# Optimization experiments

Hardware: AMD Instinct MI355X
Metric: run time of the kernel (lower is better)

The kernel has to match this reference:

```python
import jax, jax.numpy as jnp
import numpy as np

NUM_ITERS = 3

def squash(t):
    # t: [..., D]; squash along last axis exactly as the torch code:
    # sn * t / ((1+sn) * sqrt(sn))
    sn = jnp.sum(t * t, axis=-1, keepdims=True)
    return sn * t / ((1.0 + sn) * jnp.sqrt(sn))

def setup_inputs() -> dict:
    key = jax.random.key(0)
    k_x, k_w = jax.random.split(key)
    B, O, I, D_out, D_in = 512, 10, 1152, 16, 8
    x = jax.random.normal(k_x, (B, I, D_in), dtype=jnp.float32)
    W = 0.01 * jax.random.normal(k_w, (O, I, D_out, D_in), dtype=jnp.float32)
    return {"x": x, "W": W}

def reference(x, W):
    B = x.shape[0]
    O, I, D_out, _ = W.shape
    # x_hat[b,o,i,d] = sum_e W[o,i,d,e] * x[b,i,e]
    x_hat = jnp.einsum('oide,bie->boid', W, x)          # [B,O,I,D_out]
    x_hat_det = jax.lax.stop_gradient(x_hat)
    b = jnp.zeros((B, O, I), dtype=x.dtype)
    for it in range(NUM_ITERS):
        c = jax.nn.softmax(b, axis=1)                   # over out caps
        if it == NUM_ITERS - 1:
            outputs = squash(jnp.sum(c[:, :, :, None] * x_hat, axis=-2, keepdims=True))
        else:
            outputs = squash(jnp.sum(c[:, :, :, None] * x_hat_det, axis=-2, keepdims=True))
            b = b + jnp.sum(outputs * x_hat_det, axis=-1)
    outputs = jnp.squeeze(outputs, axis=-2)             # [B,O,D_out]
    # decode_idx == -1 branch: pick longest capsule
    classes = jax.nn.softmax(jnp.sqrt(jnp.sum(outputs ** 2, axis=2)), axis=1)  # [B,O]
    idx = jnp.argmax(classes, axis=1)                   # [B]
    masked = jnp.eye(O, dtype=outputs.dtype)[idx]       # [B,O]
    t = jnp.sum(outputs * masked[:, :, None], axis=1)[:, None, :]  # [B,1,D_out]
    return (t, outputs)
```

## Files before the change

kernel.cpp:

```cpp
#include <hip/hip_runtime.h>

#define BB 512
#define OO 10
#define II 1152
#define DD 16
#define EE 8
#define GB 32
#define BOD (BB * OO * DD)
#define WSLAB (II * DD * EE / 4)

typedef float v2f __attribute__((ext_vector_type(2)));
typedef float v4f __attribute__((ext_vector_type(4)));

__device__ __forceinline__ v2f pk_mul(v2f a, v2f b) {
    v2f d;
    asm("v_pk_mul_f32 %0, %1, %2" : "=v"(d) : "v"(a), "v"(b));
    return d;
}
__device__ __forceinline__ v2f pk_fma(v2f a, v2f b, v2f c) {
    v2f d;
    asm("v_pk_fma_f32 %0, %1, %2, %3" : "=v"(d) : "v"(a), "v"(b), "v"(c));
    return d;
}

__device__ __forceinline__ float dot8(v4f wa, v4f wb, v4f xa, v4f xb) {
    v2f p = pk_mul(wa.lo, xa.lo);
    p = pk_fma(wa.hi, xa.hi, p);
    p = pk_fma(wb.lo, xb.lo, p);
    p = pk_fma(wb.hi, xb.hi, p);
    return p.x + p.y;
}

template <int CTRL>
__device__ __forceinline__ float dpp_add(float v) {
    int s = __builtin_amdgcn_update_dpp(0, __float_as_int(v), CTRL, 0xf, 0xf, true);
    return v + __int_as_float(s);
}
__device__ __forceinline__ float dred16(float v) {
    v = dpp_add<0xB1>(v);
    v = dpp_add<0x4E>(v);
    v = dpp_add<0x141>(v);
    v = dpp_add<0x140>(v);
    return v;
}

__device__ __forceinline__ float squash_lane(float sv) {
    float sn = dred16(sv * sv);
    return sv * (sn / ((1.0f + sn) * sqrtf(sn)));
}

template <int PASS, int IC, int MINW, bool ATOMIC>
__global__ __launch_bounds__(256, MINW)
void caps_pass(const float* __restrict__ x, const float* __restrict__ W,
               float* __restrict__ s_out,
               const float* __restrict__ s0, const float* __restrict__ s1) {
    constexpr int ILEN = II / IC;
    constexpr int XROW = ILEN * 2 + 1;
    __shared__ v4f xlds[GB * XROW];

    const int tid = threadIdx.x;
    const int d = tid & 15;
    const int g = tid >> 4;
    const int bg = blockIdx.x & 15;
    const int ic = blockIdx.x >> 4;
    const int b0 = bg * GB + g;
    const int b1 = b0 + 16;
    const int i0 = ic * ILEN;

    const v4f* x4 = (const v4f*)x;
    for (int k = tid; k < GB * ILEN * 2; k += 256) {
        const int gg = k / (ILEN * 2);
        const int rem = k - gg * (ILEN * 2);
        xlds[gg * XROW + rem] =
            x4[(size_t)(bg * GB + gg) * (II * EE / 4) + (size_t)i0 * 2 + rem];
    }

    constexpr float LOG2E = 1.44269504f;
    float vr0[OO], vr1[OO];
    if constexpr (PASS >= 1) {
        #pragma unroll
        for (int o = 0; o < OO; o++) {
            float v = squash_lane(s0[(b0 * OO + o) * DD + d]);
            float w = squash_lane(s0[(b1 * OO + o) * DD + d]);
            if constexpr (PASS == 2) {
                v += squash_lane(s1[(b0 * OO + o) * DD + d]);
                w += squash_lane(s1[(b1 * OO + o) * DD + d]);
            }
            vr0[o] = v * LOG2E;
            vr1[o] = w * LOG2E;
        }
    }
    __syncthreads();

    float sa0[OO], sa1[OO];
    #pragma unroll
    for (int o = 0; o < OO; o++) { sa0[o] = 0.0f; sa1[o] = 0.0f; }

    const v4f* W4 = (const v4f*)W;
    int widx = (i0 * DD + d) * 2;

    for (int ii = 0; ii < ILEN; ii++) {
        const v4f xa0 = xlds[g * XROW + ii * 2 + 0];
        const v4f xb0 = xlds[g * XROW + ii * 2 + 1];
        const v4f xa1 = xlds[(g + 16) * XROW + ii * 2 + 0];
        const v4f xb1 = xlds[(g + 16) * XROW + ii * 2 + 1];

        float xh0[OO], xh1[OO];
        #pragma unroll
        for (int o = 0; o < OO; o++) {
            const v4f wa = W4[o * WSLAB + widx];
            const v4f wb = W4[o * WSLAB + widx + 1];
            xh0[o] = dot8(wa, wb, xa0, xb0);
            xh1[o] = dot8(wa, wb, xa1, xb1);
        }

        if constexpr (PASS == 0) {
            #pragma unroll
            for (int o = 0; o < OO; o++) { sa0[o] += xh0[o]; sa1[o] += xh1[o]; }
        } else {
            float e0[OO], e1[OO];
            float se0 = 0.0f, se1 = 0.0f;
            #pragma unroll
            for (int o = 0; o < OO; o++) {
                e0[o] = __builtin_amdgcn_exp2f(dred16(vr0[o] * xh0[o]));
                e1[o] = __builtin_amdgcn_exp2f(dred16(vr1[o] * xh1[o]));
                se0 += e0[o];
                se1 += e1[o];
            }
            const float inv0 = __builtin_amdgcn_rcpf(se0);
            const float inv1 = __builtin_amdgcn_rcpf(se1);
            #pragma unroll
            for (int o = 0; o < OO; o++) {
                sa0[o] = fmaf(e0[o] * inv0, xh0[o], sa0[o]);
                sa1[o] = fmaf(e1[o] * inv1, xh1[o], sa1[o]);
            }
        }
        widx += DD * 2;
    }

    if constexpr (ATOMIC) {
        const float scale = (PASS == 0) ? 0.1f : 1.0f;
        #pragma unroll
        for (int o = 0; o < OO; o++) {
            atomicAdd(&s_out[(b0 * OO + o) * DD + d], sa0[o] * scale);
            atomicAdd(&s_out[(b1 * OO + o) * DD + d], sa1[o] * scale);
        }
    } else {
        float* P = s_out + (size_t)ic * BOD;
        #pragma unroll
        for (int o = 0; o < OO; o++) {
            P[(b0 * OO + o) * DD + d] = sa0[o];
            P[(b1 * OO + o) * DD + d] = sa1[o];
        }
    }
}

template <int IC>
__global__ __launch_bounds__(256)
void caps_reduce(const float* __restrict__ P, float* __restrict__ s, float scale) {
    const int idx = blockIdx.x * 256 + threadIdx.x;
    float a = 0.0f;
    #pragma unroll 8
    for (int ic = 0; ic < IC; ic++) a += P[(size_t)ic * BOD + idx];
    s[idx] = a * scale;
}

template <int IC, bool FUSED>
__global__ __launch_bounds__(192)
void caps_final(const float* __restrict__ src, float* __restrict__ out) {
    __shared__ float norml[12];
    const int b = blockIdx.x;
    const int tid = threadIdx.x;
    const int d = tid & 15;
    const int o = tid >> 4;

    float v = 0.0f;
    if (o < OO) {
        float sv;
        const int idx = (b * OO + o) * DD + d;
        if constexpr (FUSED) {
            sv = 0.0f;
            #pragma unroll 8
            for (int ic = 0; ic < IC; ic++) sv += src[(size_t)ic * BOD + idx];
        } else {
            sv = src[idx];
        }
        const float sn = dred16(sv * sv);
        v = sv * (sn / ((1.0f + sn) * sqrtf(sn)));
        out[BB * DD + idx] = v;
        if (d == 0) norml[o] = sn;
    }
    __syncthreads();

    int idx = 0;
    float best = norml[0];
    #pragma unroll
    for (int oo = 1; oo < OO; oo++) {
        const float n = norml[oo];
        if (n > best) { best = n; idx = oo; }
    }
    if (o == idx) out[b * DD + d] = v;
}

extern "C" void kernel_launch(void* const* d_in, const int* in_sizes, int n_in,
                              void* d_out, int out_size, void* d_ws, size_t ws_size,
                              hipStream_t stream) {
    const float* x = (const float*)d_in[0];
    const float* W = (const float*)d_in[1];
    float* out = (float*)d_out;

    constexpr int ICP = 128;
    const size_t needP = ((size_t)ICP * BOD + 2 * BOD) * sizeof(float);

    if (ws_size >= needP) {
        float* P  = (float*)d_ws;
        float* s0 = P + (size_t)ICP * BOD;
        float* s1 = s0 + BOD;
        constexpr int NB = 16 * ICP;

        caps_pass<0, ICP, 4, false><<<NB, 256, 0, stream>>>(x, W, P, nullptr, nullptr);
        caps_reduce<ICP><<<BOD / 256, 256, 0, stream>>>(P, s0, 0.1f);
        caps_pass<1, ICP, 4, false><<<NB, 256, 0, stream>>>(x, W, P, s0, nullptr);
        caps_reduce<ICP><<<BOD / 256, 256, 0, stream>>>(P, s1, 1.0f);
        caps_pass<2, ICP, 4, false><<<NB, 256, 0, stream>>>(x, W, P, s0, s1);
        caps_final<ICP, true><<<BB, 192, 0, stream>>>(P, out);
    } else {
        constexpr int ICA = 64;
        float* s0 = (float*)d_ws;
        float* s1 = s0 + BOD;
        float* s2 = s1 + BOD;
        constexpr int NB = 16 * ICA;

        hipMemsetAsync(d_ws, 0, (size_t)3 * BOD * sizeof(float), stream);
        caps_pass<0, ICA, 4, true><<<NB, 256, 0, stream>>>(x, W, s0, nullptr, nullptr);
        caps_pass<1, ICA, 4, true><<<NB, 256, 0, stream>>>(x, W, s1, s0, nullptr);
        caps_pass<2, ICA, 4, true><<<NB, 256, 0, stream>>>(x, W, s2, s0, s1);
        caps_final<1, false><<<BB, 192, 0, stream>>>(s2, out);
    }
}
```

Measured before the change: 271.5 us.

## Stage W slices in LDS and read x directly from global per thread

Restructures the routing pass so each block of 512 threads stages a slice of W (6 input capsules by 10 output capsules) into shared memory in three sub-steps. Each thread handles one batch row, reading x straight from global instead of from LDS. Before, each thread covered two batch rows and read W from global while x sat in LDS. The input split is now 64 chunks of 18 capsules instead of 128 chunks of 9. This halves the partial-sum buffer and reduce traffic, and W reuse across 32 batch rows now goes through LDS. It adds extra block barriers and non-coalesced per-thread x loads.

```diff
diff --git a/kernel.cpp b/kernel.cpp
--- a/kernel.cpp
+++ b/kernel.cpp
@@ -5,9 +5,17 @@
 #define II 1152
 #define DD 16
 #define EE 8
+#define BOD (BB * OO * DD)
+#define WSLABB (II * DD * EE * 4)
+
+#define TPB 512
 #define GB 32
-#define BOD (BB * OO * DD)
-#define WSLAB (II * DD * EE / 4)
+#define ISUB 6
+#define NSUB 3
+#define ILEN (ISUB * NSUB)
+#define ICN (II / ILEN)
+#define NUNITS (OO * ISUB)
+#define WBYTES (NUNITS * 512)
 
 typedef float v2f __attribute__((ext_vector_type(2)));
 typedef float v4f __attribute__((ext_vector_type(4)));
@@ -49,109 +57,98 @@
     return sv * (sn / ((1.0f + sn) * sqrtf(sn)));
 }
 
-template <int PASS, int IC, int MINW, bool ATOMIC>
-__global__ __launch_bounds__(256, MINW)
+template <int PASS, bool ATOMIC>
+__global__ __launch_bounds__(TPB)
 void caps_pass(const float* __restrict__ x, const float* __restrict__ W,
                float* __restrict__ s_out,
                const float* __restrict__ s0, const float* __restrict__ s1) {
-    constexpr int ILEN = II / IC;
-    constexpr int XROW = ILEN * 2 + 1;
-    __shared__ v4f xlds[GB * XROW];
+    __shared__ char wlds[WBYTES];
 
     const int tid = threadIdx.x;
     const int d = tid & 15;
     const int g = tid >> 4;
     const int bg = blockIdx.x & 15;
     const int ic = blockIdx.x >> 4;
-    const int b0 = bg * GB + g;
-    const int b1 = b0 + 16;
+    const int b = bg * GB + g;
     const int i0 = ic * ILEN;
 
-    const v4f* x4 = (const v4f*)x;
-    for (int k = tid; k < GB * ILEN * 2; k += 256) {
-        const int gg = k / (ILEN * 2);
-        const int rem = k - gg * (ILEN * 2);
-        xlds[gg * XROW + rem] =
-            x4[(size_t)(bg * GB + gg) * (II * EE / 4) + (size_t)i0 * 2 + rem];
-    }
-
     constexpr float LOG2E = 1.44269504f;
-    float vr0[OO], vr1[OO];
+    float vr[OO];
     if constexpr (PASS >= 1) {
         #pragma unroll
         for (int o = 0; o < OO; o++) {
-            float v = squash_lane(s0[(b0 * OO + o) * DD + d]);
-            float w = squash_lane(s0[(b1 * OO + o) * DD + d]);
-            if constexpr (PASS == 2) {
-                v += squash_lane(s1[(b0 * OO + o) * DD + d]);
-                w += squash_lane(s1[(b1 * OO + o) * DD + d]);
+            float v = squash_lane(s0[(b * OO + o) * DD + d]);
+            if constexpr (PASS == 2) v += squash_lane(s1[(b * OO + o) * DD + d]);
+            vr[o] = v * LOG2E;
+        }
+    }
+
+    float sacc[OO];
+    #pragma unroll
+    for (int o = 0; o < OO; o++) sacc[o] = 0.0f;
+
+    const char* xrow = (const char*)x + ((size_t)b * II + i0) * (EE * 4);
+
+    for (int s = 0; s < NSUB; s++) {
+        if (s) __syncthreads();
+        {
+            const char* Wg = (const char*)W + (size_t)(i0 + s * ISUB) * 512;
+            for (int k = tid; k < NUNITS * 32; k += TPB) {
+                const int u  = k >> 5;
+                const int o  = u / ISUB;
+                const int ii = u - o * ISUB;
+                const int sl = k & 31;
+                const v4f w = *(const v4f*)(Wg + (size_t)o * WSLABB + ii * 512
+                                            + (sl & 15) * 32 + (sl >> 4) * 16);
+                *(v4f*)(wlds + k * 16) = w;
             }
-            vr0[o] = v * LOG2E;
-            vr1[o] = w * LOG2E;
-        }
-    }
-    __syncthreads();
-
-    float sa0[OO], sa1[OO];
-    #pragma unroll
-    for (int o = 0; o < OO; o++) { sa0[o] = 0.0f; sa1[o] = 0.0f; }
-
-    const v4f* W4 = (const v4f*)W;
-    int widx = (i0 * DD + d) * 2;
-
-    for (int ii = 0; ii < ILEN; ii++) {
-        const v4f xa0 = xlds[g * XROW + ii * 2 + 0];
-        const v4f xb0 = xlds[g * XROW + ii * 2 + 1];
-        const v4f xa1 = xlds[(g + 16) * XROW + ii * 2 + 0];
-        const v4f xb1 = xlds[(g + 16) * XROW + ii * 2 + 1];
-
-        float xh0[OO], xh1[OO];
-        #pragma unroll
-        for (int o = 0; o < OO; o++) {
-            const v4f wa = W4[o * WSLAB + widx];
-            const v4f wb = W4[o * WSLAB + widx + 1];
-            xh0[o] = dot8(wa, wb, xa0, xb0);
-            xh1[o] = dot8(wa, wb, xa1, xb1);
-        }
-
-        if constexpr (PASS == 0) {
-            #pragma unroll
-            for (int o = 0; o < OO; o++) { sa0[o] += xh0[o]; sa1[o] += xh1[o]; }
-        } else {
-            float e0[OO], e1[OO];
-            float se0 = 0.0f, se1 = 0.0f;
+        }
+        __syncthreads();
+
+        const char* xs = xrow + s * ISUB * 32;
+        const char* wd = wlds + (d << 4);
+        #pragma unroll
+        for (int ii = 0; ii < ISUB; ii++) {
+            const v4f xa = *(const v4f*)(xs + ii * 32);
+            const v4f xb = *(const v4f*)(xs + ii * 32 + 16);
+
+            float xh[OO];
             #pragma unroll
             for (int o = 0; o < OO; o++) {
-                e0[o] = __builtin_amdgcn_exp2f(dred16(vr0[o] * xh0[o]));
-                e1[o] = __builtin_amdgcn_exp2f(dred16(vr1[o] * xh1[o]));
-                se0 += e0[o];
-                se1 += e1[o];
+                const v4f wa = *(const v4f*)(wd + (o * ISUB + ii) * 512);
+                const v4f wb = *(const v4f*)(wd + (o * ISUB + ii) * 512 + 256);
+                xh[o] = dot8(wa, wb, xa, xb);
             }
-            const float inv0 = __builtin_amdgcn_rcpf(se0);
-            const float inv1 = __builtin_amdgcn_rcpf(se1);
-            #pragma unroll
-            for (int o = 0; o < OO; o++) {
-                sa0[o] = fmaf(e0[o] * inv0, xh0[o], sa0[o]);
-                sa1[o] = fmaf(e1[o] * inv1, xh1[o], sa1[o]);
+
+            if constexpr (PASS == 0) {
+                #pragma unroll
+                for (int o = 0; o < OO; o++) sacc[o] += xh[o];
+            } else {
+                float e[OO];
+                float se = 0.0f;
+                #pragma unroll
+                for (int o = 0; o < OO; o++) {
+                    e[o] = __builtin_amdgcn_exp2f(dred16(vr[o] * xh[o]));
+                    se += e[o];
+                }
+                const float inv = __builtin_amdgcn_rcpf(se);
+                #pragma unroll
+                for (int o = 0; o < OO; o++)
+                    sacc[o] = fmaf(e[o] * inv, xh[o], sacc[o]);
             }
         }
-        widx += DD * 2;
     }
 
     if constexpr (ATOMIC) {
         const float scale = (PASS == 0) ? 0.1f : 1.0f;
         #pragma unroll
-        for (int o = 0; o < OO; o++) {
-            atomicAdd(&s_out[(b0 * OO + o) * DD + d], sa0[o] * scale);
-            atomicAdd(&s_out[(b1 * OO + o) * DD + d], sa1[o] * scale);
-        }
+        for (int o = 0; o < OO; o++)
+            atomicAdd(&s_out[(b * OO + o) * DD + d], sacc[o] * scale);
     } else {
         float* P = s_out + (size_t)ic * BOD;
         #pragma unroll
-        for (int o = 0; o < OO; o++) {
-            P[(b0 * OO + o) * DD + d] = sa0[o];
-            P[(b1 * OO + o) * DD + d] = sa1[o];
-        }
+        for (int o = 0; o < OO; o++)
+            P[(b * OO + o) * DD + d] = sacc[o];
     }
 }
 
@@ -209,32 +206,29 @@
     const float* W = (const float*)d_in[1];
     float* out = (float*)d_out;
 
-    constexpr int ICP = 128;
-    const size_t needP = ((size_t)ICP * BOD + 2 * BOD) * sizeof(float);
+    constexpr int NB = 16 * ICN;
+    const size_t needP = ((size_t)ICN * BOD + 2 * BOD) * sizeof(float);
 
     if (ws_size >= needP) {
         float* P  = (float*)d_ws;
-        float* s0 = P + (size_t)ICP * BOD;
+        float* s0 = P + (size_t)ICN * BOD;
         float* s1 = s0 + BOD;
-        constexpr int NB = 16 * ICP;
-
-        caps_pass<0, ICP, 4, false><<<NB, 256, 0, stream>>>(x, W, P, nullptr, nullptr);
-        caps_reduce<ICP><<<BOD / 256, 256, 0, stream>>>(P, s0, 0.1f);
-        caps_pass<1, ICP, 4, false><<<NB, 256, 0, stream>>>(x, W, P, s0, nullptr);
-        caps_reduce<ICP><<<BOD / 256, 256, 0, stream>>>(P, s1, 1.0f);
-        caps_pass<2, ICP, 4, false><<<NB, 256, 0, stream>>>(x, W, P, s0, s1);
-        caps_final<ICP, true><<<BB, 192, 0, stream>>>(P, out);
+
+        caps_pass<0, false><<<NB, TPB, 0, stream>>>(x, W, P, nullptr, nullptr);
+        caps_reduce<ICN><<<BOD / 256, 256, 0, stream>>>(P, s0, 0.1f);
+        caps_pass<1, false><<<NB, TPB, 0, stream>>>(x, W, P, s0, nullptr);
+        caps_reduce<ICN><<<BOD / 256, 256, 0, stream>>>(P, s1, 1.0f);
+        caps_pass<2, false><<<NB, TPB, 0, stream>>>(x, W, P, s0, s1);
+        caps_final<ICN, true><<<BB, 192, 0, stream>>>(P, out);
     } else {
-        constexpr int ICA = 64;
         float* s0 = (float*)d_ws;
         float* s1 = s0 + BOD;
         float* s2 = s1 + BOD;
-        constexpr int NB = 16 * ICA;
 
         hipMemsetAsync(d_ws, 0, (size_t)3 * BOD * sizeof(float), stream);
-        caps_pass<0, ICA, 4, true><<<NB, 256, 0, stream>>>(x, W, s0, nullptr, nullptr);
-        caps_pass<1, ICA, 4, true><<<NB, 256, 0, stream>>>(x, W, s1, s0, nullptr);
-        caps_pass<2, ICA, 4, true><<<NB, 256, 0, stream>>>(x, W, s2, s0, s1);
+        caps_pass<0, true><<<NB, TPB, 0, stream>>>(x, W, s0, nullptr, nullptr);
+        caps_pass<1, true><<<NB, TPB, 0, stream>>>(x, W, s1, s0, nullptr);
+        caps_pass<2, true><<<NB, TPB, 0, stream>>>(x, W, s2, s0, s1);
         caps_final<1, false><<<BB, 192, 0, stream>>>(s2, out);
     }
 }
```

Result: no change. 266.4 us (-1.9%).
